# Performance work log

Hardware: AMD Instinct MI355X
Metric: run time of the kernel (lower is better)

The kernel has to match this reference:

```python
import jax, jax.numpy as jnp
import numpy as np

B, S, D, H, NH, C = 32, 512, 768, 768, 4, 10
HD = H // NH


def _lin(x, w, b):
    return x @ w.T + b


def _ln(x, g, b, eps=1e-5):
    mu = jnp.mean(x, axis=-1, keepdims=True)
    var = jnp.mean(jnp.square(x - mu), axis=-1, keepdims=True)
    return (x - mu) * jax.lax.rsqrt(var + eps) * g + b


def setup_inputs() -> dict:
    key = jax.random.key(0)
    ks = jax.random.split(key, 16)
    w = lambda k, shape: jax.random.normal(k, shape, dtype=jnp.float32) * 0.02
    return {
        "x": jax.random.normal(ks[0], (B, S, D), dtype=jnp.float32),
        "wq": w(ks[1], (H, D)), "bq": jnp.zeros((H,), jnp.float32),
        "wk": w(ks[2], (H, D)), "bk": jnp.zeros((H,), jnp.float32),
        "wv": w(ks[3], (H, D)), "bv": jnp.zeros((H,), jnp.float32),
        "wx": w(ks[4], (H, D)), "bx": jnp.zeros((H,), jnp.float32),
        "in_proj_w": w(ks[5], (3 * H, H)), "in_proj_b": jnp.zeros((3 * H,), jnp.float32),
        "out_proj_w": w(ks[6], (H, H)), "out_proj_b": jnp.zeros((H,), jnp.float32),
        "fc1a_w": w(ks[7], (H, H)), "fc1a_b": jnp.zeros((H,), jnp.float32),
        "fc1b_w": w(ks[8], (H, H)), "fc1b_b": jnp.zeros((H,), jnp.float32),
        "ln_g": jnp.ones((H,), jnp.float32), "ln_b": jnp.zeros((H,), jnp.float32),
        "fc2_w": w(ks[9], (C, H)), "fc2_b": jnp.zeros((C,), jnp.float32),
    }


def reference(x, wq, bq, wk, bk, wv, bv, wx, bx, in_proj_w, in_proj_b,
              out_proj_w, out_proj_b, fc1a_w, fc1a_b, fc1b_w, fc1b_b,
              ln_g, ln_b, fc2_w, fc2_b):
    # Vectorized sinusoidal PE matching the triple loop:
    # even i: sin(pos / 10000^(2i/D)); odd i: cos(pos / 10000^(2(i-1)/D))
    d = x.shape[2]
    pos = jnp.arange(x.shape[1], dtype=x.dtype)[:, None]          # [S,1]
    i = jnp.arange(d)
    i_even = (i - (i % 2)).astype(x.dtype)                        # 2*(i - i%2)/d exponent
    angle = pos / jnp.power(jnp.asarray(10000.0, x.dtype), 2.0 * i_even / d)  # [S,D]
    pe = jnp.where(i % 2 == 0, jnp.sin(angle), jnp.cos(angle))
    x = x + pe[None]

    q = _lin(x, wq, bq)
    k = _lin(x, wk, bk)
    v = _lin(x, wv, bv)
    xr = _lin(x, wx, bx)

    # torch MultiheadAttention: in_proj, split heads, SDPA, out_proj
    wq_i, wk_i, wv_i = jnp.split(in_proj_w, 3, axis=0)
    bq_i, bk_i, bv_i = jnp.split(in_proj_b, 3, axis=0)
    b = x.shape[0]
    q2 = _lin(q, wq_i, bq_i).reshape(b, -1, NH, HD)
    k2 = _lin(k, wk_i, bk_i).reshape(b, -1, NH, HD)
    v2 = _lin(v, wv_i, bv_i).reshape(b, -1, NH, HD)
    scores = jnp.einsum('bqhd,bkhd->bhqk', q2, k2) / jnp.sqrt(jnp.asarray(HD, x.dtype))
    attn = jax.nn.softmax(scores, axis=-1)
    ctx = jnp.einsum('bhqk,bkhd->bqhd', attn, v2).reshape(b, -1, H)
    attn_out = _lin(ctx, out_proj_w, out_proj_b)

    x = _ln(xr + attn_out, ln_g, ln_b)
    ffn = _lin(jax.nn.relu(_lin(x, fc1a_w, fc1a_b)), fc1b_w, fc1b_b)
    x = _ln(x + ffn, ln_g, ln_b)
    x = jnp.sum(x, axis=1)
    return _lin(x, fc2_w, fc2_b)
```

## Files before the change

### kernel.cpp

```cpp
#include <hip/hip_runtime.h>
#include <hip/hip_bf16.h>

typedef __bf16 bf16;
typedef __bf16 bf16x8 __attribute__((ext_vector_type(8)));
typedef __bf16 bf16x4 __attribute__((ext_vector_type(4)));
typedef __bf16 bf16x2 __attribute__((ext_vector_type(2)));
typedef float  f32x4  __attribute__((ext_vector_type(4)));

#define GLD16(g, l) __builtin_amdgcn_global_load_lds(                        \
    (const __attribute__((address_space(1))) void*)(g),                      \
    (__attribute__((address_space(3))) void*)(l), 16, 0, 0)

template<int BM, int BN, int MFR, int NFR>
__global__ __launch_bounds__(256, 3)
void gemm_nt(const bf16* __restrict__ A, const bf16* __restrict__ B,
             bf16* __restrict__ C, const float* __restrict__ bias,
             int K, int lda, int ldb, int ldc,
             int inner,
             long long aOut, long long aIn,
             long long bOut, long long bIn,
             long long cOut, long long cIn,
             float alpha, int relu,
             const bf16* __restrict__ res, int ldr)
{
    const int z  = blockIdx.z;
    const int zo = z / inner;
    const int zi = z - zo * inner;
    A += (long long)zo * aOut + (long long)zi * aIn;
    B += (long long)zo * bOut + (long long)zi * bIn;
    C += (long long)zo * cOut + (long long)zi * cIn;

    const int tm = blockIdx.y * BM;
    const int tn = blockIdx.x * BN;

    __shared__ __align__(16) bf16 smem[(BM + BN) * 64];
    bf16* As = smem;
    bf16* Bs = smem + BM * 64;

    const int tid  = threadIdx.x;
    const int lane = tid & 63;
    const int wid  = tid >> 6;
    const int wr   = wid >> 1;
    const int wc   = wid & 1;

    f32x4 acc[MFR][NFR];
#pragma unroll
    for (int i = 0; i < MFR; ++i)
#pragma unroll
        for (int j = 0; j < NFR; ++j) acc[i][j] = (f32x4){0.f, 0.f, 0.f, 0.f};

    const int srow = lane >> 3;
    const int gch8 = ((lane & 7) ^ srow) * 8;

    const int NA = BM / 32;
    const int NB = BN / 32;

    const bf16* aP[NA];
#pragma unroll
    for (int jj = 0; jj < NA; ++jj) {
        const int R0 = (wid * NA + jj) * 8;
        aP[jj] = A + (long long)(tm + R0 + srow) * lda + gch8;
    }
    const bf16* bP[NB];
#pragma unroll
    for (int jj = 0; jj < NB; ++jj) {
        const int R0 = (wid * NB + jj) * 8;
        bP[jj] = B + (long long)(tn + R0 + srow) * ldb + gch8;
    }

    const int lr = lane & 15;
    const int qg = lane >> 4;

    for (int kt = 0; kt < K; kt += 64) {
#pragma unroll
        for (int jj = 0; jj < NA; ++jj)
            GLD16(aP[jj], As + (wid * NA + jj) * 512);
#pragma unroll
        for (int jj = 0; jj < NB; ++jj)
            GLD16(bP[jj], Bs + (wid * NB + jj) * 512);
        __syncthreads();

#pragma unroll
        for (int h = 0; h < 2; ++h) {
            const int off = ((qg + h * 4) ^ (lr & 7)) * 8;
            bf16x8 af[MFR], bfr[NFR];
#pragma unroll
            for (int i = 0; i < MFR; ++i)
                af[i] = *(const bf16x8*)(As + (wr * MFR * 16 + i * 16 + lr) * 64 + off);
#pragma unroll
            for (int j = 0; j < NFR; ++j)
                bfr[j] = *(const bf16x8*)(Bs + (wc * NFR * 16 + j * 16 + lr) * 64 + off);
#pragma unroll
            for (int i = 0; i < MFR; ++i)
#pragma unroll
                for (int j = 0; j < NFR; ++j)
                    acc[i][j] = __builtin_amdgcn_mfma_f32_16x16x32_bf16(
                        af[i], bfr[j], acc[i][j], 0, 0, 0);
        }
        __syncthreads();
#pragma unroll
        for (int jj = 0; jj < NA; ++jj) aP[jj] += 64;
#pragma unroll
        for (int jj = 0; jj < NB; ++jj) bP[jj] += 64;
    }

#pragma unroll
    for (int i = 0; i < MFR; ++i) {
#pragma unroll
        for (int j = 0; j < NFR; ++j) {
            const int mm0 = tm + wr * MFR * 16 + i * 16 + (lane >> 4) * 4;
            const int nn  = tn + wc * NFR * 16 + j * 16 + (lane & 15);
#pragma unroll
            for (int r = 0; r < 4; ++r) {
                float v = acc[i][j][r] * alpha;
                if (bias) v += bias[nn];
                if (res)  v += (float)res[(long long)(mm0 + r) * ldr + nn];
                if (relu) v = fmaxf(v, 0.f);
                C[(long long)(mm0 + r) * ldc + nn] = (bf16)v;
            }
        }
    }
}

#define BAR8()  __builtin_amdgcn_s_barrier()
#define LGKM0() do { asm volatile("s_waitcnt lgkmcnt(0)" ::: "memory");      \
                     __builtin_amdgcn_sched_barrier(0); } while (0)

#define RD_A(S, MB)                                                          \
    _Pragma("unroll") for (int mi = 0; mi < 4; ++mi)                         \
    _Pragma("unroll") for (int h = 0; h < 2; ++h)                            \
        af[mi][h] = *(const bf16x8*)((S) + aBase + ((MB) + mi) * 1024 +      \
                                     (h ? koff1 : koff0));

#define RD_B(S, NJ)                                                          \
    _Pragma("unroll") for (int h = 0; h < 2; ++h)                            \
        bfv[NJ][h] = *(const bf16x8*)((S) + bBase + (NJ) * 1024 +            \
                                      (h ? koff1 : koff0));

#define MFMA_Q(MB, N0, N1)                                                   \
    __builtin_amdgcn_s_setprio(1);                                          \
    _Pragma("unroll") for (int h = 0; h < 2; ++h)                            \
    _Pragma("unroll") for (int mi = 0; mi < 4; ++mi) {                       \
        acc[(MB)+mi][(N0)] = __builtin_amdgcn_mfma_f32_16x16x32_bf16(        \
            af[mi][h], bfv[(N0)][h], acc[(MB)+mi][(N0)], 0, 0, 0);           \
        acc[(MB)+mi][(N1)] = __builtin_amdgcn_mfma_f32_16x16x32_bf16(        \
            af[mi][h], bfv[(N1)][h], acc[(MB)+mi][(N1)], 0, 0, 0);           \
    }                                                                        \
    __builtin_amdgcn_s_setprio(0);

#define STAGE8(DST)                                                          \
    _Pragma("unroll") for (int jj = 0; jj < 4; ++jj)                         \
        GLD16(aP[jj], (DST) + (wid * 4 + jj) * 512);                         \
    _Pragma("unroll") for (int jj = 0; jj < 4; ++jj)                         \
        GLD16(bP[jj], (DST) + 16384 + (wid * 4 + jj) * 512);                 \
    _Pragma("unroll") for (int jj = 0; jj < 4; ++jj) { aP[jj] += 64; bP[jj] += 64; }

#define K_TILE(S, DO_STAGE, SYNC)                                            \
  {                                                                          \
    RD_A((S), 0); RD_B((S), 0); RD_B((S), 1);                                \
    BAR8(); LGKM0();                                                         \
    MFMA_Q(0, 0, 1)                                                          \
    BAR8();                                                                  \
    RD_B((S), 2); RD_B((S), 3);                                              \
    BAR8(); LGKM0();                                                         \
    MFMA_Q(0, 2, 3)                                                          \
    BAR8();                                                                  \
    RD_A((S), 4);                                                            \
    BAR8(); LGKM0();                                                         \
    MFMA_Q(4, 2, 3)                                                          \
    BAR8();                                                                  \
    if (DO_STAGE) { STAGE8((S)) }                                            \
    BAR8();                                                                  \
    MFMA_Q(4, 0, 1)                                                          \
    if ((SYNC) == 0) asm volatile("s_waitcnt vmcnt(8)" ::: "memory");        \
    if ((SYNC) == 1) asm volatile("s_waitcnt vmcnt(0)" ::: "memory");        \
    if ((SYNC) != 2) BAR8();                                                 \
  }

__global__ __launch_bounds__(512, 2)
void gemm_qkv_8ph(const bf16* __restrict__ A, const bf16* __restrict__ B,
                  bf16* __restrict__ C, const float* __restrict__ bias)
{
    constexpr int LDA = 768, LDB = 768, LDC = 3072;
    const int tm = blockIdx.y * 256;
    const int tn = blockIdx.x * 256;

    __shared__ __align__(16) bf16 smem[2][2 * 256 * 64];

    const int tid  = threadIdx.x;
    const int lane = tid & 63;
    const int wid  = tid >> 6;
    const int wr   = wid >> 2;
    const int wc   = wid & 3;
    const int lr   = lane & 15;
    const int qg   = lane >> 4;

    const int srow = lane >> 3;
    const int gch8 = ((lane & 7) ^ srow) * 8;
    const bf16* aP[4];
    const bf16* bP[4];
#pragma unroll
    for (int jj = 0; jj < 4; ++jj) {
        aP[jj] = A + (long long)(tm + wid * 32 + jj * 8 + srow) * LDA + gch8;
        bP[jj] = B + (long long)(tn + wid * 32 + jj * 8 + srow) * LDB + gch8;
    }

    f32x4 acc[8][4];
#pragma unroll
    for (int i = 0; i < 8; ++i)
#pragma unroll
        for (int j = 0; j < 4; ++j) acc[i][j] = (f32x4){0.f, 0.f, 0.f, 0.f};

    const int aBase = (wr * 128 + lr) * 64;
    const int bBase = 16384 + (wc * 64 + lr) * 64;
    const int koff0 = ((qg    ) ^ (lr & 7)) * 8;
    const int koff1 = ((qg + 4) ^ (lr & 7)) * 8;

    bf16x8 af[4][2];
    bf16x8 bfv[4][2];

    bf16* S0 = &smem[0][0];
    bf16* S1 = &smem[1][0];

    STAGE8(S0)
    STAGE8(S1)
    asm volatile("s_waitcnt vmcnt(8)" ::: "memory");
    BAR8();

#pragma unroll 1
    for (int it = 0; it < 5; ++it) {
        K_TILE(S0, 1, 0)
        K_TILE(S1, 1, 0)
    }
    K_TILE(S0, 0, 1)
    K_TILE(S1, 0, 2)

    float bv[4];
#pragma unroll
    for (int j = 0; j < 4; ++j) bv[j] = bias[tn + wc * 64 + j * 16 + lr];

#pragma unroll
    for (int i = 0; i < 8; ++i) {
        const int mm0 = tm + wr * 128 + i * 16 + qg * 4;
#pragma unroll
        for (int j = 0; j < 4; ++j) {
            const int nn = tn + wc * 64 + j * 16 + lr;
#pragma unroll
            for (int r = 0; r < 4; ++r)
                C[(long long)(mm0 + r) * LDC + nn] = (bf16)(acc[i][j][r] + bv[j]);
        }
    }
}

__global__ __launch_bounds__(256, 2)
void fused_attn_kernel(bf16* __restrict__ qkvx)
{
    const int flat = blockIdx.x;
    const int qt = (flat >> 3) & 3;
    const int z  = (flat & 7) | ((flat >> 5) << 3);
    const int b  = z >> 2, h = z & 3;

    const bf16* Qg = qkvx + (long long)b * 512 * 3072 + h * 192;
    const bf16* Kg = Qg + 768;
    const bf16* Vg = Qg + 1536;

    __shared__ __align__(16) bf16 Ks[64 * 192];
    __shared__ __align__(16) bf16 VTs[192 * 64];
    __shared__ __align__(16) bf16 Pb[4 * 32 * 64];

    const int tid  = threadIdx.x;
    const int lane = tid & 63;
    const int wid  = tid >> 6;
    const int lr   = lane & 15;
    const int qg   = lane >> 4;
    const int m0   = qt * 128 + wid * 32;

    bf16x8 qf[2][6];
#pragma unroll
    for (int mt = 0; mt < 2; ++mt)
#pragma unroll
        for (int t = 0; t < 6; ++t)
            qf[mt][t] = *(const bf16x8*)(Qg + (long long)(m0 + mt * 16 + lr) * 3072
                                         + t * 32 + qg * 8);

    const bf16* kP[6];
#pragma unroll
    for (int i = 0; i < 6; ++i) {
        const int c = i * 256 + tid;
        const int krow = c / 24, kcc = c % 24;
        const int kgc  = (kcc & 24) | ((kcc & 7) ^ (krow & 7));
        kP[i] = Kg + (long long)krow * 3072 + kgc * 8;
    }
    const int vkp = tid & 31;
    const int vdc = tid >> 5;

    f32x4 acc[2][12];
#pragma unroll
    for (int mt = 0; mt < 2; ++mt)
#pragma unroll
        for (int dt = 0; dt < 12; ++dt) acc[mt][dt] = (f32x4){0.f, 0.f, 0.f, 0.f};
    float mrow[2][4], lrow[2][4];
#pragma unroll
    for (int mt = 0; mt < 2; ++mt)
#pragma unroll
        for (int r = 0; r < 4; ++r) { mrow[mt][r] = -3e38f; lrow[mt][r] = 0.f; }

    const float alpha = 0.0721687836f;

    for (int kt = 0; kt < 8; ++kt) {
#pragma unroll
        for (int i = 0; i < 6; ++i)
            GLD16(kP[i], Ks + (i * 256 + wid * 64) * 8);
#pragma unroll
        for (int i = 0; i < 3; ++i) {
            const int dc = vdc + i * 8;
            const bf16* p = Vg + (long long)(2 * vkp) * 3072 + dc * 8;
            const bf16x8 v0 = *(const bf16x8*)(p);
            const bf16x8 v1 = *(const bf16x8*)(p + 3072);
#pragma unroll
            for (int j = 0; j < 8; ++j) {
                const int d = dc * 8 + j;
                bf16x2 pk; pk[0] = v0[j]; pk[1] = v1[j];
                *(bf16x2*)(VTs + d * 64 + ((vkp >> 2) ^ (d & 7)) * 8
                           + 2 * (vkp & 3)) = pk;
            }
        }
        __syncthreads();

        f32x4 sf[2][4];
#pragma unroll
        for (int mt = 0; mt < 2; ++mt)
#pragma unroll
            for (int nt = 0; nt < 4; ++nt) sf[mt][nt] = (f32x4){0.f, 0.f, 0.f, 0.f};
#pragma unroll
        for (int nt = 0; nt < 4; ++nt) {
#pragma unroll
            for (int t = 0; t < 6; ++t) {
                const int ch = t * 4 + qg;
                const int ph = (ch & 24) | ((ch & 7) ^ (lr & 7));
                const bf16x8 kf = *(const bf16x8*)(Ks + (nt * 16 + lr) * 192 + ph * 8);
                sf[0][nt] = __builtin_amdgcn_mfma_f32_16x16x32_bf16(qf[0][t], kf, sf[0][nt], 0, 0, 0);
                sf[1][nt] = __builtin_amdgcn_mfma_f32_16x16x32_bf16(qf[1][t], kf, sf[1][nt], 0, 0, 0);
            }
        }

#pragma unroll
        for (int mt = 0; mt < 2; ++mt) {
            float mx[4], a[4], rs[4], p[4][4];
#pragma unroll
            for (int r = 0; r < 4; ++r) {
                float v0 = fmaxf(sf[mt][0][r], sf[mt][1][r]);
                float v1 = fmaxf(sf[mt][2][r], sf[mt][3][r]);
                mx[r] = fmaxf(v0, v1) * alpha;
            }
#pragma unroll
            for (int msk = 1; msk <= 8; msk <<= 1)
#pragma unroll
                for (int r = 0; r < 4; ++r) mx[r] = fmaxf(mx[r], __shfl_xor(mx[r], msk));
#pragma unroll
            for (int r = 0; r < 4; ++r) {
                const float mn = fmaxf(mrow[mt][r], mx[r]);
                a[r] = __expf(mrow[mt][r] - mn);
                mrow[mt][r] = mn;
                rs[r] = 0.f;
            }
#pragma unroll
            for (int nt = 0; nt < 4; ++nt)
#pragma unroll
                for (int r = 0; r < 4; ++r) {
                    p[nt][r] = __expf(sf[mt][nt][r] * alpha - mrow[mt][r]);
                    rs[r] += p[nt][r];
                }
#pragma unroll
            for (int msk = 1; msk <= 8; msk <<= 1)
#pragma unroll
                for (int r = 0; r < 4; ++r) rs[r] += __shfl_xor(rs[r], msk);
#pragma unroll
            for (int r = 0; r < 4; ++r) lrow[mt][r] = lrow[mt][r] * a[r] + rs[r];
#pragma unroll
            for (int dt = 0; dt < 12; ++dt)
#pragma unroll
                for (int r = 0; r < 4; ++r) acc[mt][dt][r] *= a[r];
#pragma unroll
            for (int nt = 0; nt < 4; ++nt)
#pragma unroll
                for (int r = 0; r < 4; ++r) {
                    const int row = mt * 16 + qg * 4 + r;
                    const int ph2 = (nt * 2 + (lr >> 3)) ^ (row & 7);
                    Pb[wid * 2048 + row * 64 + ph2 * 8 + (lr & 7)] = (bf16)p[nt][r];
                }
        }

        bf16x8 pf[2][2];
#pragma unroll
        for (int mt = 0; mt < 2; ++mt)
#pragma unroll
            for (int ks = 0; ks < 2; ++ks) {
                const int row = mt * 16 + lr;
                const int ph  = (ks * 4 + qg) ^ (lr & 7);
                pf[mt][ks] = *(const bf16x8*)(Pb + wid * 2048 + row * 64 + ph * 8);
            }
#pragma unroll
        for (int dt = 0; dt < 12; ++dt) {
#pragma unroll
            for (int ks = 0; ks < 2; ++ks) {
                const int ph = (ks * 4 + qg) ^ (lr & 7);
                const bf16x8 vf = *(const bf16x8*)(VTs + (dt * 16 + lr) * 64 + ph * 8);
                acc[0][dt] = __builtin_amdgcn_mfma_f32_16x16x32_bf16(pf[0][ks], vf, acc[0][dt], 0, 0, 0);
                acc[1][dt] = __builtin_amdgcn_mfma_f32_16x16x32_bf16(pf[1][ks], vf, acc[1][dt], 0, 0, 0);
            }
        }
        __syncthreads();
#pragma unroll
        for (int i = 0; i < 6; ++i) kP[i] += 64 * 3072;
        Vg += 64 * 3072;
    }

    bf16* Og = qkvx + (long long)b * 512 * 3072 + h * 192;
#pragma unroll
    for (int mt = 0; mt < 2; ++mt) {
        float inv[4];
#pragma unroll
        for (int r = 0; r < 4; ++r) inv[r] = 1.0f / lrow[mt][r];
#pragma unroll
        for (int dt = 0; dt < 12; ++dt)
#pragma unroll
            for (int r = 0; r < 4; ++r) {
                const int row = m0 + mt * 16 + qg * 4 + r;
                Og[(long long)row * 3072 + dt * 16 + lr] = (bf16)(acc[mt][dt][r] * inv[r]);
            }
    }
}

__device__ __forceinline__ void cast4(const float* src, bf16* dst, int i)
{
    const float4 v = *(const float4*)(src + (long long)i * 4);
    bf16x4 o;
    o[0] = (bf16)v.x; o[1] = (bf16)v.y; o[2] = (bf16)v.z; o[3] = (bf16)v.w;
    *(bf16x4*)(dst + (long long)i * 4) = o;
}

__global__ __launch_bounds__(256)
void prep_kernel(const float* __restrict__ wq, const float* __restrict__ wk,
                 const float* __restrict__ wv, const float* __restrict__ wx,
                 const float* __restrict__ inpw, const float* __restrict__ inpb,
                 const float* __restrict__ bq, const float* __restrict__ bk,
                 const float* __restrict__ bv, const float* __restrict__ bx,
                 const float* __restrict__ woutp, const float* __restrict__ wf1a,
                 const float* __restrict__ wf1b, const float* __restrict__ x,
                 bf16* __restrict__ WT3, bf16* __restrict__ INPJ,
                 bf16* __restrict__ WOUT, bf16* __restrict__ WF1A,
                 bf16* __restrict__ WF1B, bf16* __restrict__ WXD,
                 float* __restrict__ BCAT, bf16* __restrict__ XPE)
{
    const int blk = blockIdx.x;
    const int tid = threadIdx.x;
    __shared__ bf16 t[32][33];

    if (blk < 1728) {
        const int which = blk / 576, local = blk - which * 576;
        const float* src = (which == 0) ? wq : ((which == 1) ? wk : wv);
        bf16* dst = WT3 + (long long)which * 589824;
        const int r0 = (local / 24) * 32, c0 = (local % 24) * 32;
        const int tr = tid >> 5, tc = tid & 31;
#pragma unroll
        for (int k = 0; k < 4; ++k) {
            const int r = tr + k * 8;
            t[r][tc] = (bf16)src[(long long)(r0 + r) * 768 + c0 + tc];
        }
        __syncthreads();
#pragma unroll
        for (int k = 0; k < 4; ++k) {
            const int c = tr + k * 8;
            dst[(long long)(c0 + c) * 768 + r0 + tc] = t[tc][c];
        }
    } else if (blk < 3456) {
        cast4(inpw, INPJ, (blk - 1728) * 256 + tid);
    } else if (blk < 4032) {
        cast4(woutp, WOUT, (blk - 3456) * 256 + tid);
    } else if (blk < 4608) {
        cast4(wf1a, WF1A, (blk - 4032) * 256 + tid);
    } else if (blk < 5184) {
        cast4(wf1b, WF1B, (blk - 4608) * 256 + tid);
    } else if (blk < 5760) {
        cast4(wx, WXD, (blk - 5184) * 256 + tid);
    } else if (blk < 6051) {
        const int bl = blk - 5760;
        if (bl < 288) {
            const int g = tid >> 5, l = tid & 31;
            const int n = bl * 8 + g;
            const int zsec = n / 768;
            const float* bb = (zsec == 0) ? bq : ((zsec == 1) ? bk : bv);
            const float* wrow = inpw + (long long)n * 768;
            float s = 0.f;
            for (int d = l; d < 768; d += 32) s += wrow[d] * bb[d];
#pragma unroll
            for (int off = 16; off; off >>= 1) s += __shfl_xor(s, off);
            if (l == 0) BCAT[n] = inpb[n] + s;
        } else {
            const int n = (bl - 288) * 256 + tid;
            if (n < 768) BCAT[2304 + n] = bx[n];
        }
    } else {
        const int idx4 = ((blk - 6051) * 256 + tid) * 4;
        const int d    = idx4 % 768;
        const int row  = idx4 / 768;
        const int s    = row & 511;
        const float ksc = -0.034603417655076f;
        const float4 xv = *(const float4*)(x + (long long)idx4);
        float a0 = (float)s * exp2f((float)d * ksc);
        float a1 = (float)s * exp2f((float)(d + 2) * ksc);
        float s0, c0, s1, c1;
        sincosf(a0, &s0, &c0);
        sincosf(a1, &s1, &c1);
        bf16x4 o;
        o[0] = (bf16)(xv.x + s0);
        o[1] = (bf16)(xv.y + c0);
        o[2] = (bf16)(xv.z + s1);
        o[3] = (bf16)(xv.w + c1);
        *(bf16x4*)(XPE + (long long)idx4) = o;
    }
}

__global__ __launch_bounds__(192)
void ln1_kernel(const bf16* __restrict__ a, int lda_,
                bf16* __restrict__ o, int ldo,
                const float* __restrict__ g, const float* __restrict__ be)
{
    const int row = blockIdx.x;
    const int t   = threadIdx.x;
    const int d0  = t * 4;
    const bf16x4 av = *(const bf16x4*)(a + (long long)row * lda_ + d0);
    float xv[4];
#pragma unroll
    for (int k = 0; k < 4; ++k) xv[k] = (float)av[k];
    float s1 = xv[0] + xv[1] + xv[2] + xv[3];
    float s2 = xv[0]*xv[0] + xv[1]*xv[1] + xv[2]*xv[2] + xv[3]*xv[3];
    for (int off = 32; off; off >>= 1) {
        s1 += __shfl_xor(s1, off);
        s2 += __shfl_xor(s2, off);
    }
    __shared__ float red[6];
    const int wid = t >> 6, lane = t & 63;
    if (lane == 0) { red[wid] = s1; red[3 + wid] = s2; }
    __syncthreads();
    s1 = red[0] + red[1] + red[2];
    s2 = red[3] + red[4] + red[5];
    const float mu  = s1 * (1.0f / 768.0f);
    const float var = s2 * (1.0f / 768.0f) - mu * mu;
    const float rs  = rsqrtf(var + 1e-5f);
    const float4 gv = *(const float4*)(g + d0);
    const float4 ev = *(const float4*)(be + d0);
    bf16x4 ov;
    ov[0] = (bf16)(((xv[0] - mu) * rs) * gv.x + ev.x);
    ov[1] = (bf16)(((xv[1] - mu) * rs) * gv.y + ev.y);
    ov[2] = (bf16)(((xv[2] - mu) * rs) * gv.z + ev.z);
    ov[3] = (bf16)(((xv[3] - mu) * rs) * gv.w + ev.w);
    *(bf16x4*)(o + (long long)row * ldo + d0) = ov;
}

__global__ __launch_bounds__(256)
void ln2_reduce_kernel(const bf16* __restrict__ src,
                       const float* __restrict__ g, const float* __restrict__ be,
                       float* __restrict__ partial)
{
    const int blk  = blockIdx.x;
    const int tid  = threadIdx.x;
    const int wid  = tid >> 6, lane = tid & 63;
    const int d0   = lane * 12;

    float gv[12], ev[12];
#pragma unroll
    for (int k = 0; k < 12; k += 4) {
        *(float4*)(gv + k) = *(const float4*)(g + d0 + k);
        *(float4*)(ev + k) = *(const float4*)(be + d0 + k);
    }
    float acc[12];
#pragma unroll
    for (int k = 0; k < 12; ++k) acc[k] = 0.f;

    for (int i = 0; i < 8; ++i) {
        const int row = blk * 32 + i * 4 + wid;
        const bf16* p = src + (long long)row * 3072 + d0;
        float xv[12];
#pragma unroll
        for (int k = 0; k < 12; k += 4) {
            const bf16x4 v = *(const bf16x4*)(p + k);
            xv[k] = (float)v[0]; xv[k+1] = (float)v[1];
            xv[k+2] = (float)v[2]; xv[k+3] = (float)v[3];
        }
        float s1 = 0.f, s2 = 0.f;
#pragma unroll
        for (int k = 0; k < 12; ++k) { s1 += xv[k]; s2 += xv[k] * xv[k]; }
        for (int off = 32; off; off >>= 1) {
            s1 += __shfl_xor(s1, off);
            s2 += __shfl_xor(s2, off);
        }
        const float mu  = s1 * (1.0f / 768.0f);
        const float var = s2 * (1.0f / 768.0f) - mu * mu;
        const float rs  = rsqrtf(var + 1e-5f);
#pragma unroll
        for (int k = 0; k < 12; ++k) acc[k] += (xv[k] - mu) * rs * gv[k] + ev[k];
    }

    __shared__ float red[4][768];
#pragma unroll
    for (int k = 0; k < 12; k += 4)
        *(float4*)(&red[wid][d0 + k]) = *(const float4*)(acc + k);
    __syncthreads();
    if (wid == 0) {
#pragma unroll
        for (int k = 0; k < 12; k += 4) {
            const float4 a0 = *(const float4*)(&red[0][d0 + k]);
            const float4 a1 = *(const float4*)(&red[1][d0 + k]);
            const float4 a2 = *(const float4*)(&red[2][d0 + k]);
            const float4 a3 = *(const float4*)(&red[3][d0 + k]);
            *(float4*)(partial + (long long)blk * 768 + d0 + k) =
                make_float4(a0.x + a1.x + a2.x + a3.x, a0.y + a1.y + a2.y + a3.y,
                            a0.z + a1.z + a2.z + a3.z, a0.w + a1.w + a2.w + a3.w);
        }
    }
}

__global__ __launch_bounds__(192)
void reduce_fc2_stage2_kernel(const float* __restrict__ partial, const float* __restrict__ w,
                              const float* __restrict__ bias, float* __restrict__ out)
{
    const int b = blockIdx.x, t = threadIdx.x;
    const int d0 = t * 4;
    float a[4] = {0.f, 0.f, 0.f, 0.f};
    for (int c = 0; c < 16; ++c) {
        const float4 pv = *(const float4*)(partial + (long long)(b * 16 + c) * 768 + d0);
        a[0] += pv.x; a[1] += pv.y; a[2] += pv.z; a[3] += pv.w;
    }
    __shared__ float os[10];
    if (t < 10) os[t] = 0.f;
    __syncthreads();
    for (int c = 0; c < 10; ++c) {
        const float4 wv = *(const float4*)(w + c * 768 + d0);
        float p = wv.x * a[0] + wv.y * a[1] + wv.z * a[2] + wv.w * a[3];
        for (int off = 32; off; off >>= 1) p += __shfl_xor(p, off);
        if ((t & 63) == 0) atomicAdd(&os[c], p);
    }
    __syncthreads();
    if (t < 10) out[b * 10 + t] = os[t] + bias[t];
}

static const size_t OFF_XPE  = 0;
static const size_t OFF_WCAT = OFF_XPE  + (size_t)16384 * 768 * 2;
static const size_t OFF_WT3  = OFF_WCAT + (size_t)3072 * 768 * 2;
static const size_t OFF_INPJ = OFF_WT3  + (size_t)3 * 768 * 768 * 2;
static const size_t OFF_WOUT = OFF_INPJ + (size_t)2304 * 768 * 2;
static const size_t OFF_WF1A = OFF_WOUT + (size_t)768 * 768 * 2;
static const size_t OFF_WF1B = OFF_WF1A + (size_t)768 * 768 * 2;
static const size_t OFF_BCAT = OFF_WF1B + (size_t)768 * 768 * 2;
static const size_t OFF_QKVX = OFF_BCAT + (size_t)3072 * 4;
static const size_t OFF_VT   = OFF_QKVX + (size_t)16384 * 3072 * 2;
static const size_t OFF_S    = OFF_VT   + (size_t)128 * 192 * 512 * 2;
static const size_t OFF_X1   = OFF_S    + (size_t)128 * 512 * 512 * 2;

extern "C" void kernel_launch(void* const* d_in, const int* in_sizes, int n_in,
                              void* d_out, int out_size, void* d_ws, size_t ws_size,
                              hipStream_t stream)
{
    const float* x     = (const float*)d_in[0];
    const float* wq    = (const float*)d_in[1];
    const float* bq    = (const float*)d_in[2];
    const float* wk    = (const float*)d_in[3];
    const float* bk    = (const float*)d_in[4];
    const float* wv    = (const float*)d_in[5];
    const float* bv    = (const float*)d_in[6];
    const float* wx    = (const float*)d_in[7];
    const float* bx    = (const float*)d_in[8];
    const float* inpw  = (const float*)d_in[9];
    const float* inpb  = (const float*)d_in[10];
    const float* woutp = (const float*)d_in[11];
    const float* boutp = (const float*)d_in[12];
    const float* wf1a  = (const float*)d_in[13];
    const float* bf1a  = (const float*)d_in[14];
    const float* wf1b  = (const float*)d_in[15];
    const float* bf1b  = (const float*)d_in[16];
    const float* lng   = (const float*)d_in[17];
    const float* lnb   = (const float*)d_in[18];
    const float* wfc2  = (const float*)d_in[19];
    const float* bfc2  = (const float*)d_in[20];
    float* out = (float*)d_out;

    char* ws = (char*)d_ws;
    bf16*  XPE  = (bf16*)(ws + OFF_XPE);
    bf16*  WCAT = (bf16*)(ws + OFF_WCAT);
    bf16*  WT3  = (bf16*)(ws + OFF_WT3);
    bf16*  INPJ = (bf16*)(ws + OFF_INPJ);
    bf16*  WOUT = (bf16*)(ws + OFF_WOUT);
    bf16*  WF1A = (bf16*)(ws + OFF_WF1A);
    bf16*  WF1B = (bf16*)(ws + OFF_WF1B);
    float* BCAT = (float*)(ws + OFF_BCAT);
    bf16*  QKVX = (bf16*)(ws + OFF_QKVX);
    float* PART = (float*)(ws + OFF_S);
    bf16*  X1   = (bf16*)(ws + OFF_X1);

    prep_kernel<<<18339, 256, 0, stream>>>(wq, wk, wv, wx, inpw, inpb,
                                           bq, bk, bv, bx, woutp, wf1a, wf1b, x,
                                           WT3, INPJ, WOUT, WF1A, WF1B,
                                           WCAT + (size_t)2304 * 768, BCAT, XPE);

    gemm_nt<64, 128, 2, 4><<<dim3(6, 12, 3), 256, 0, stream>>>(
        INPJ, WT3, WCAT, nullptr, 768, 768, 768, 768,
        1, 589824, 0, 589824, 0, 589824, 0, 1.0f, 0, nullptr, 0);

    gemm_qkv_8ph<<<dim3(12, 64, 1), 512, 0, stream>>>(XPE, WCAT, QKVX, BCAT);

    fused_attn_kernel<<<512, 256, 0, stream>>>(QKVX);

    gemm_nt<64, 128, 2, 4><<<dim3(6, 256, 1), 256, 0, stream>>>(
        QKVX, WOUT, QKVX + 768, boutp, 768, 3072, 768, 3072,
        1, 0, 0, 0, 0, 0, 0, 1.0f, 0, QKVX + 2304, 3072);

    ln1_kernel<<<16384, 192, 0, stream>>>(QKVX + 768, 3072, X1, 768, lng, lnb);

    gemm_nt<64, 128, 2, 4><<<dim3(6, 256, 1), 256, 0, stream>>>(
        X1, WF1A, QKVX + 1536, bf1a, 768, 768, 768, 3072,
        1, 0, 0, 0, 0, 0, 0, 1.0f, 1, nullptr, 0);

    gemm_nt<64, 128, 2, 4><<<dim3(6, 256, 1), 256, 0, stream>>>(
        QKVX + 1536, WF1B, QKVX + 2304, bf1b, 768, 3072, 768, 3072,
        1, 0, 0, 0, 0, 0, 0, 1.0f, 0, X1, 768);

    ln2_reduce_kernel<<<512, 256, 0, stream>>>(QKVX + 2304, lng, lnb, PART);

    reduce_fc2_stage2_kernel<<<32, 192, 0, stream>>>(PART, wfc2, bfc2, out);
}
```

Baseline: 491.6 us.

## Restructure QKV GEMM pipeline: prefetch next tile during compute, drop ping-pong barriers

The 8-phase QKV GEMM previously staged two tiles up front and used many intra-tile barriers. Now only one tile is prefetched, and the next tile's A and B loads are issued interleaved with LDS reads and MFMA of the current tile. Only one barrier per K tile remains, after a full vmcnt(0) wait. This cuts barrier overhead but reduces prefetch depth to a single tile, which may expose global load latency.

New measurement: 475.4 us. -3.3%, faster.

```diff
diff --git a/kernel.cpp b/kernel.cpp
--- a/kernel.cpp
+++ b/kernel.cpp
@@ -148,33 +148,30 @@
     }                                                                        \
     __builtin_amdgcn_s_setprio(0);
 
-#define STAGE8(DST)                                                          \
-    _Pragma("unroll") for (int jj = 0; jj < 4; ++jj)                         \
-        GLD16(aP[jj], (DST) + (wid * 4 + jj) * 512);                         \
-    _Pragma("unroll") for (int jj = 0; jj < 4; ++jj)                         \
-        GLD16(bP[jj], (DST) + 16384 + (wid * 4 + jj) * 512);                 \
-    _Pragma("unroll") for (int jj = 0; jj < 4; ++jj) { aP[jj] += 64; bP[jj] += 64; }
-
-#define K_TILE(S, DO_STAGE, SYNC)                                            \
+#define STAGE_A(DST)                                                         \
+    _Pragma("unroll") for (int jj = 0; jj < 4; ++jj) {                       \
+        GLD16(aP[jj], (DST) + (wid * 4 + jj) * 512);  aP[jj] += 64; }
+
+#define STAGE_B(DST)                                                         \
+    _Pragma("unroll") for (int jj = 0; jj < 4; ++jj) {                       \
+        GLD16(bP[jj], (DST) + 16384 + (wid * 4 + jj) * 512);  bP[jj] += 64; }
+
+#define K_TILE_F(CUR, NXT, STG, LAST)                                        \
   {                                                                          \
-    RD_A((S), 0); RD_B((S), 0); RD_B((S), 1);                                \
-    BAR8(); LGKM0();                                                         \
+    RD_A((CUR), 0); RD_B((CUR), 0); RD_B((CUR), 1);                          \
+    if (STG) { STAGE_A(NXT) }                                                \
+    LGKM0();                                                                 \
     MFMA_Q(0, 0, 1)                                                          \
-    BAR8();                                                                  \
-    RD_B((S), 2); RD_B((S), 3);                                              \
-    BAR8(); LGKM0();                                                         \
+    RD_B((CUR), 2); RD_B((CUR), 3);                                          \
+    if (STG) { STAGE_B(NXT) }                                                \
+    LGKM0();                                                                 \
     MFMA_Q(0, 2, 3)                                                          \
-    BAR8();                                                                  \
-    RD_A((S), 4);                                                            \
-    BAR8(); LGKM0();                                                         \
+    RD_A((CUR), 4);                                                          \
+    LGKM0();                                                                 \
     MFMA_Q(4, 2, 3)                                                          \
-    BAR8();                                                                  \
-    if (DO_STAGE) { STAGE8((S)) }                                            \
-    BAR8();                                                                  \
     MFMA_Q(4, 0, 1)                                                          \
-    if ((SYNC) == 0) asm volatile("s_waitcnt vmcnt(8)" ::: "memory");        \
-    if ((SYNC) == 1) asm volatile("s_waitcnt vmcnt(0)" ::: "memory");        \
-    if ((SYNC) != 2) BAR8();                                                 \
+    if (!(LAST)) { asm volatile("s_waitcnt vmcnt(0)" ::: "memory");          \
+                   __builtin_amdgcn_sched_barrier(0); BAR8(); }              \
   }
 
 __global__ __launch_bounds__(512, 2)
@@ -222,18 +219,18 @@
     bf16* S0 = &smem[0][0];
     bf16* S1 = &smem[1][0];
 
-    STAGE8(S0)
-    STAGE8(S1)
-    asm volatile("s_waitcnt vmcnt(8)" ::: "memory");
+    STAGE_A(S0)
+    STAGE_B(S0)
+    asm volatile("s_waitcnt vmcnt(0)" ::: "memory");
     BAR8();
 
 #pragma unroll 1
     for (int it = 0; it < 5; ++it) {
-        K_TILE(S0, 1, 0)
-        K_TILE(S1, 1, 0)
-    }
-    K_TILE(S0, 0, 1)
-    K_TILE(S1, 0, 2)
+        K_TILE_F(S0, S1, 1, 0)
+        K_TILE_F(S1, S0, 1, 0)
+    }
+    K_TILE_F(S0, S1, 1, 0)
+    K_TILE_F(S1, S0, 0, 1)
 
     float bv[4];
 #pragma unroll
```
